# Performance work log

Measured on AMD Instinct MI355X. Metric: run time of the kernel, lower is better.

The kernel has to match this reference:

```python
import jax, jax.numpy as jnp
import numpy as np

B, S, D, H = 64, 1024, 128, 256  # batch, seq, input_dim, hidden_dim


def _glorot(key, shape):
    fan_in, fan_out = shape[0], shape[-1]
    lim = np.sqrt(6.0 / (fan_in + fan_out)).astype(np.float32)
    return jax.random.uniform(key, shape, jnp.float32, -lim, lim)


def setup_inputs() -> dict:
    key = jax.random.key(0)
    ks = jax.random.split(key, 13)
    inp = {
        "x": jax.random.normal(ks[0], (B, S, D), jnp.float32),
        # forward-direction lite-GRU params
        "Wz_f": _glorot(ks[1], (D, H)), "Uz_f": _glorot(ks[2], (H, H)), "bz_f": jnp.zeros((H,), jnp.float32),
        "Wh_f": _glorot(ks[3], (D, H)), "Uh_f": _glorot(ks[4], (H, H)), "bh_f": jnp.zeros((H,), jnp.float32),
        # backward-direction lite-GRU params
        "Wz_b": _glorot(ks[5], (D, H)), "Uz_b": _glorot(ks[6], (H, H)), "bz_b": jnp.zeros((H,), jnp.float32),
        "Wh_b": _glorot(ks[7], (D, H)), "Uh_b": _glorot(ks[8], (H, H)), "bh_b": jnp.zeros((H,), jnp.float32),
        # attention: Linear(2H,2H) -> Tanh -> Linear(2H,1) -> Softmax(dim=1)
        "W1": _glorot(ks[9], (2 * H, 2 * H)), "b1": jnp.zeros((2 * H,), jnp.float32),
        "w2": _glorot(ks[10], (2 * H, 1)), "b2": jnp.zeros((1,), jnp.float32),
    }
    return inp


def _lite_gru(x, Wz, Uz, bz, Wh, Uh, bh):
    # x: [B,S,D] -> outputs [B,S,H]; lite GRU (no reset gate)
    xz = jnp.einsum('bsd,dh->bsh', x, Wz) + bz  # precompute input projections
    xh = jnp.einsum('bsd,dh->bsh', x, Wh) + bh

    def step(h, inps):
        xz_t, xh_t = inps  # [B,H]
        z = jax.nn.sigmoid(xz_t + h @ Uz)
        hc = jnp.tanh(xh_t + h @ Uh)
        h = z * h + (1.0 - z) * hc
        return h, h

    h0 = jnp.zeros((x.shape[0], Uz.shape[0]), x.dtype)
    _, ys = jax.lax.scan(step, h0, (jnp.swapaxes(xz, 0, 1), jnp.swapaxes(xh, 0, 1)))
    return jnp.swapaxes(ys, 0, 1)  # [B,S,H]


def reference(x, Wz_f, Uz_f, bz_f, Wh_f, Uh_f, bh_f,
              Wz_b, Uz_b, bz_b, Wh_b, Uh_b, bh_b, W1, b1, w2, b2):
    out_f = _lite_gru(x, Wz_f, Uz_f, bz_f, Wh_f, Uh_f, bh_f)
    out_b = _lite_gru(x[:, ::-1, :], Wz_b, Uz_b, bz_b, Wh_b, Uh_b, bh_b)[:, ::-1, :]
    out = jnp.concatenate([out_f, out_b], axis=-1)  # [B,S,2H]
    # additive attention: Linear -> tanh -> Linear -> softmax over time
    scores = jnp.tanh(out @ W1 + b1) @ w2 + b2       # [B,S,1]
    attn = jax.nn.softmax(scores, axis=1)
    context = jnp.sum(attn * out, axis=1)            # [B,2H]
    return context
```

## Files before the change

### kernel.cpp

```cpp
#include <hip/hip_runtime.h>
#include <cstdint>
#include <cstddef>

typedef _Float16 f16;
typedef _Float16 f16x8 __attribute__((ext_vector_type(8)));
typedef _Float16 f16x4 __attribute__((ext_vector_type(4)));
typedef _Float16 f16x2 __attribute__((ext_vector_type(2)));
typedef float f32x4 __attribute__((ext_vector_type(4)));

#define MFMA16(a, b, c) __builtin_amdgcn_mfma_f32_16x16x32_f16((a), (b), (c), 0, 0, 0)


static constexpr size_t UT_OFF  = 0;
static constexpr size_t WT_OFF  = 524288;
static constexpr size_t W1T_OFF = 786432;
static constexpr size_t XP_OFF  = 1310720;
static constexpr size_t OUT_OFF = XP_OFF + 134217728;
static constexpr size_t SC_OFF  = OUT_OFF + 67108864;
static constexpr size_t AT_OFF  = SC_OFF + 262144;
static constexpr size_t PART_OFF= AT_OFF + 262144;

#define SCALE_Z 1.4426950408889634f
#define SCALE_H 2.8853900817779268f

__device__ __forceinline__ float fexp2(float x) {
#if __has_builtin(__builtin_amdgcn_exp2f)
    return __builtin_amdgcn_exp2f(x);
#else
    return __expf(x * 0.6931471805599453f);
#endif
}

__global__ void k0_prep(const float* __restrict__ Uzf, const float* __restrict__ Uhf,
                        const float* __restrict__ Uzb, const float* __restrict__ Uhb,
                        const float* __restrict__ Wzf, const float* __restrict__ Whf,
                        const float* __restrict__ Wzb, const float* __restrict__ Whb,
                        const float* __restrict__ W1,
                        f16* __restrict__ Ut, f16* __restrict__ Wt, f16* __restrict__ W1t)
{
    int tid = blockIdx.x * blockDim.x + threadIdx.x;
    int nthr = gridDim.x * blockDim.x;
    for (int i = tid; i < 4 * 256 * 256; i += nthr) {
        int u = i >> 16, cc = (i >> 8) & 255, k = i & 255;
        const float* U = (u == 0) ? Uzf : (u == 1) ? Uhf : (u == 2) ? Uzb : Uhb;
        float sg = (u & 1) ? SCALE_H : SCALE_Z;
        Ut[i] = (f16)(U[k * 256 + cc] * sg);
    }
    for (int i = tid; i < 2 * 512 * 128; i += nthr) {
        int dir = i >> 16, cc2 = (i >> 7) & 511, k = i & 127;
        const float* W = dir ? ((cc2 & 256) ? Whb : Wzb) : ((cc2 & 256) ? Whf : Wzf);
        Wt[i] = (f16)W[k * 256 + (cc2 & 255)];
    }
    for (int i = tid; i < 512 * 512; i += nthr) {
        int n = i >> 9, k = i & 511;
        W1t[i] = (f16)W1[k * 512 + n];
    }
}

__launch_bounds__(256, 2)
__global__ void k1_xproj(const float* __restrict__ x, const f16* __restrict__ Wt,
                         const float* __restrict__ bzf, const float* __restrict__ bhf,
                         const float* __restrict__ bzb, const float* __restrict__ bhb,
                         f16* __restrict__ xp2)
{
    int bid = blockIdx.x;
    int s = bid & 1023, g = (bid >> 10) & 3, dir = bid >> 12;
    int s_src = dir ? (1023 - s) : s;
    int tid = threadIdx.x, w = tid >> 6, lane = tid & 63, q = lane >> 4, l16 = lane & 15;

    f16x8 bf[4];
    const float* xr = x + ((size_t)(g * 16 + l16) * 1024 + s_src) * 128;
#pragma unroll
    for (int kt = 0; kt < 4; ++kt) {
        int k0 = kt * 32 + q * 8;
        f32x4 a = *(const f32x4*)(xr + k0);
        f32x4 c = *(const f32x4*)(xr + k0 + 4);
        f16x8 v;
#pragma unroll
        for (int j = 0; j < 4; ++j) { v[j] = (f16)a[j]; v[4 + j] = (f16)c[j]; }
        bf[kt] = v;
    }
    const f16* wt = Wt + (size_t)dir * 512 * 128;
    f16x8 af[8][4];
#pragma unroll
    for (int mt = 0; mt < 8; ++mt) {
        int cc2 = w * 128 + mt * 16 + l16;
#pragma unroll
        for (int kt = 0; kt < 4; ++kt)
            af[mt][kt] = *(const f16x8*)(wt + cc2 * 128 + kt * 32 + q * 8);
    }
    f32x4 acc[8];
#pragma unroll
    for (int mt = 0; mt < 8; ++mt) acc[mt] = (f32x4){0.f, 0.f, 0.f, 0.f};
#pragma unroll
    for (int kt = 0; kt < 4; ++kt)
#pragma unroll
        for (int mt = 0; mt < 8; ++mt)
            acc[mt] = MFMA16(af[mt][kt], bf[kt], acc[mt]);

    f16* dst = xp2 + (size_t)((dir * 4 + g) * 1024 + s) * 8192;
#pragma unroll
    for (int mt = 0; mt < 8; ++mt) {
        int ccg = w * 128 + mt * 16 + q * 4;
        int gate = ccg >> 8, c = ccg & 255;
        const float* bias = gate ? (dir ? bhb : bhf) : (dir ? bzb : bzf);
        float sg = gate ? SCALE_H : SCALE_Z;
        f32x4 bi = *(const f32x4*)(bias + c);
        f16x4 o;
#pragma unroll
        for (int r = 0; r < 4; ++r) o[r] = (f16)((acc[mt][r] + bi[r]) * sg);
        int flat = ((gate * 2 + ((c >> 4) & 1)) * 8 + (c >> 5)) * 256 + (q * 16 + l16) * 4;
        *(f16x4*)(dst + flat) = o;
    }
}

#define GRU_STEP(P, SS, CX)                                                   \
    {                                                                         \
        const int cur = (P), nxt = (P) ^ 1;                                   \
        f16x8 bf[8];                                                          \
        _Pragma("unroll")                                                     \
        for (int j = 0; j < 8; ++j)                                           \
            bf[j] = *(const f16x8*)&h16[cur][l16][j * 32 + q * 8];            \
        f32x4 acc[4];                                                         \
        _Pragma("unroll")                                                     \
        for (int t = 0; t < 4; ++t)                                           \
            _Pragma("unroll")                                                 \
            for (int r = 0; r < 4; ++r) acc[t][r] = (float)CX[t][r];          \
        int sp = (SS) + 2; if (sp > 1023) sp = 1023;                          \
        const f16* px = xb + (size_t)sp * 8192;                               \
        _Pragma("unroll")                                                     \
        for (int t = 0; t < 4; ++t) CX[t] = *(const f16x4*)(px + offs[t]);    \
        _Pragma("unroll")                                                     \
        for (int j = 0; j < 8; ++j)                                           \
            _Pragma("unroll")                                                 \
            for (int t = 0; t < 4; ++t)                                       \
                acc[t] = MFMA16(uf[t][j], bf[j], acc[t]);                     \
        _Pragma("unroll")                                                     \
        for (int p = 0; p < 2; ++p) {                                         \
            f32x4 hn; f16x4 hh;                                               \
            _Pragma("unroll")                                                 \
            for (int r = 0; r < 4; ++r) {                                     \
                float az = acc[p][r];                                         \
                float ah = acc[2 + p][r];                                     \
                float E1 = fexp2(-az);                                        \
                float E2 = fexp2(-ah);                                        \
                float h0 = hold[p][r];                                        \
                float num = __builtin_fmaf(h0, E2, h0)                        \
                          + __builtin_fmaf(-E1, E2, E1);                      \
                float den = (1.f + E1) * (1.f + E2);                          \
                float hv = num * __builtin_amdgcn_rcpf(den);                  \
                hn[r] = hv; hh[r] = (f16)hv;                                  \
            }                                                                 \
            hold[p] = hn;                                                     \
            int ccg = w * 32 + p * 16 + q * 4;                                \
            *(f16x4*)&h16[nxt][l16][ccg] = hh;                                \
            *(f16x4*)(op + p * 16) = hh;                                      \
        }                                                                     \
        op += sstep;                                                          \
        asm volatile("s_waitcnt lgkmcnt(0)" ::: "memory");                    \
        __builtin_amdgcn_s_barrier();                                         \
        asm volatile("" ::: "memory");                                        \
    }

__launch_bounds__(512, 2)
__global__ void k2_gru(const f16* __restrict__ Ut, const f16* __restrict__ xp2,
                       f16* __restrict__ out16)
{
    int bid = blockIdx.x;
    int dir = bid >> 2, g = bid & 3;
    int tid = threadIdx.x, w = tid >> 6, lane = tid & 63, q = lane >> 4, l16 = lane & 15;

    __shared__ f16 h16[2][16][264];

    for (int i = tid; i < 2 * 16 * 264; i += 512) (&h16[0][0][0])[i] = (f16)0.f;

    f16x8 uf[4][8];
#pragma unroll
    for (int t = 0; t < 4; ++t) {
        int gate = t >> 1;
        int cc = w * 32 + (t & 1) * 16 + l16;
        const f16* up = Ut + ((size_t)(dir * 2 + gate) * 256 + cc) * 256;
#pragma unroll
        for (int j = 0; j < 8; ++j)
            uf[t][j] = *(const volatile f16x8*)(up + j * 32 + q * 8);
    }

    const f16* xb = xp2 + (size_t)(dir * 4 + g) * 1024 * 8192;
    int offs[4];
#pragma unroll
    for (int t = 0; t < 4; ++t) {
        int gate = t >> 1, p = t & 1;
        offs[t] = ((gate * 2 + p) * 8 + w) * 256 + lane * 4;
    }
    f16x4 cxA[4], cxB[4];
#pragma unroll
    for (int t = 0; t < 4; ++t) cxA[t] = *(const f16x4*)(xb + offs[t]);
#pragma unroll
    for (int t = 0; t < 4; ++t) cxB[t] = *(const f16x4*)(xb + 8192 + offs[t]);

    f32x4 hold[2];
    hold[0] = (f32x4){0.f, 0.f, 0.f, 0.f};
    hold[1] = (f32x4){0.f, 0.f, 0.f, 0.f};

    f16* op = out16 + ((size_t)(g * 16 + l16) * 1024 + (dir ? 1023 : 0)) * 512
            + dir * 256 + w * 32 + q * 4;
    ptrdiff_t sstep = dir ? -512 : 512;

    __syncthreads();

    for (int s = 0; s < 1024; s += 2) {
        GRU_STEP(0, s, cxA)
        GRU_STEP(1, s + 1, cxB)
    }
}

__launch_bounds__(256, 2)
__global__ void k3_scores(const f16* __restrict__ out16, const f16* __restrict__ W1t,
                          const float* __restrict__ b1, const float* __restrict__ w2,
                          const float* __restrict__ b2, float* __restrict__ scores)
{
    int bid = blockIdx.x;
    int b = bid >> 4, sc = bid & 15, s0 = sc * 64;
    int tid = threadIdx.x, w = tid >> 6, lane = tid & 63, q = lane >> 4, l16 = lane & 15;
    f32x4 acc[4][8];
#pragma unroll
    for (int mt = 0; mt < 4; ++mt)
#pragma unroll
        for (int nt = 0; nt < 8; ++nt) acc[mt][nt] = (f32x4){0.f, 0.f, 0.f, 0.f};

    for (int kt = 0; kt < 16; ++kt) {
        f16x8 af[4];
#pragma unroll
        for (int mt = 0; mt < 4; ++mt) {
            size_t row = (size_t)b * 1024 + s0 + mt * 16 + l16;
            af[mt] = *(const f16x8*)(out16 + row * 512 + kt * 32 + q * 8);
        }
        f16x8 bfg[8];
#pragma unroll
        for (int nt = 0; nt < 8; ++nt) {
            int ncol = w * 128 + nt * 16 + l16;
            bfg[nt] = *(const f16x8*)(W1t + (size_t)ncol * 512 + kt * 32 + q * 8);
        }
#pragma unroll
        for (int mt = 0; mt < 4; ++mt)
#pragma unroll
            for (int nt = 0; nt < 8; ++nt)
                acc[mt][nt] = MFMA16(af[mt], bfg[nt], acc[mt][nt]);
    }
    float b1v[8], w2v[8];
#pragma unroll
    for (int nt = 0; nt < 8; ++nt) {
        int ncol = w * 128 + nt * 16 + l16;
        b1v[nt] = b1[ncol];
        w2v[nt] = w2[ncol];
    }
    __shared__ float spart[4][64];
    float rs[4][4];
#pragma unroll
    for (int mt = 0; mt < 4; ++mt)
#pragma unroll
        for (int r = 0; r < 4; ++r) {
            float ssum = 0.f;
#pragma unroll
            for (int nt = 0; nt < 8; ++nt) {
                float xv = acc[mt][nt][r] + b1v[nt];
                float t = 1.f - 2.f / (1.f + __expf(2.f * xv));
                ssum += t * w2v[nt];
            }
            rs[mt][r] = ssum;
        }
#pragma unroll
    for (int off = 1; off < 16; off <<= 1)
#pragma unroll
        for (int mt = 0; mt < 4; ++mt)
#pragma unroll
            for (int r = 0; r < 4; ++r)
                rs[mt][r] += __shfl_xor(rs[mt][r], off, 64);
    if (l16 == 0) {
#pragma unroll
        for (int mt = 0; mt < 4; ++mt)
#pragma unroll
            for (int r = 0; r < 4; ++r)
                spart[w][mt * 16 + q * 4 + r] = rs[mt][r];
    }
    __syncthreads();
    if (tid < 64) {
        float v = spart[0][tid] + spart[1][tid] + spart[2][tid] + spart[3][tid] + b2[0];
        scores[b * 1024 + s0 + tid] = v;
    }
}

__global__ void k3_softmax(const float* __restrict__ scores, float* __restrict__ attn)
{
    int b = blockIdx.x, tid = threadIdx.x;
    __shared__ float red[4];
    f32x4 v = *(const f32x4*)(scores + b * 1024 + tid * 4);
    float m = fmaxf(fmaxf(v[0], v[1]), fmaxf(v[2], v[3]));
#pragma unroll
    for (int off = 1; off < 64; off <<= 1) m = fmaxf(m, __shfl_xor(m, off, 64));
    if ((tid & 63) == 0) red[tid >> 6] = m;
    __syncthreads();
    m = fmaxf(fmaxf(red[0], red[1]), fmaxf(red[2], red[3]));
    __syncthreads();
    float e0 = __expf(v[0] - m), e1 = __expf(v[1] - m), e2 = __expf(v[2] - m), e3 = __expf(v[3] - m);
    float ssum = e0 + e1 + e2 + e3;
#pragma unroll
    for (int off = 1; off < 64; off <<= 1) ssum += __shfl_xor(ssum, off, 64);
    if ((tid & 63) == 0) red[tid >> 6] = ssum;
    __syncthreads();
    float inv = 1.f / (red[0] + red[1] + red[2] + red[3]);
    f32x4 o = {e0 * inv, e1 * inv, e2 * inv, e3 * inv};
    *(f32x4*)(attn + b * 1024 + tid * 4) = o;
}

__global__ void k3_wsum(const f16* __restrict__ out16, const float* __restrict__ attn,
                        float* __restrict__ part)
{
    int bid = blockIdx.x;
    int b = bid >> 3, ch = bid & 7;
    int tid = threadIdx.x;
    const f16* op = out16 + ((size_t)b * 1024 + ch * 128) * 512 + tid * 2;
    const float* ap = attn + b * 1024 + ch * 128;
    float a0 = 0.f, a1 = 0.f;
#pragma unroll 4
    for (int i = 0; i < 128; ++i) {
        float aw = ap[i];
        f16x2 xv = *(const f16x2*)(op + (size_t)i * 512);
        a0 += aw * (float)xv[0];
        a1 += aw * (float)xv[1];
    }
    part[(size_t)(b * 8 + ch) * 512 + tid * 2] = a0;
    part[(size_t)(b * 8 + ch) * 512 + tid * 2 + 1] = a1;
}

__global__ void k3_final(const float* __restrict__ part, float* __restrict__ outp)
{
    int b = blockIdx.x, tid = threadIdx.x;
#pragma unroll
    for (int j = 0; j < 2; ++j) {
        int cc = tid * 2 + j;
        float ssum = 0.f;
#pragma unroll
        for (int ch = 0; ch < 8; ++ch) ssum += part[(size_t)(b * 8 + ch) * 512 + cc];
        outp[b * 512 + cc] = ssum;
    }
}

extern "C" void kernel_launch(void* const* d_in, const int* in_sizes, int n_in,
                              void* d_out, int out_size, void* d_ws, size_t ws_size,
                              hipStream_t stream)
{
    const float* x   = (const float*)d_in[0];
    const float* Wzf = (const float*)d_in[1];
    const float* Uzf = (const float*)d_in[2];
    const float* bzf = (const float*)d_in[3];
    const float* Whf = (const float*)d_in[4];
    const float* Uhf = (const float*)d_in[5];
    const float* bhf = (const float*)d_in[6];
    const float* Wzb = (const float*)d_in[7];
    const float* Uzb = (const float*)d_in[8];
    const float* bzb = (const float*)d_in[9];
    const float* Whb = (const float*)d_in[10];
    const float* Uhb = (const float*)d_in[11];
    const float* bhb = (const float*)d_in[12];
    const float* W1  = (const float*)d_in[13];
    const float* b1  = (const float*)d_in[14];
    const float* w2  = (const float*)d_in[15];
    const float* b2  = (const float*)d_in[16];
    float* outp = (float*)d_out;

    char* ws = (char*)d_ws;
    f16* Ut    = (f16*)(ws + UT_OFF);
    f16* Wt    = (f16*)(ws + WT_OFF);
    f16* W1t   = (f16*)(ws + W1T_OFF);
    f16* xp2   = (f16*)(ws + XP_OFF);
    f16* o16   = (f16*)(ws + OUT_OFF);
    float* sc  = (float*)(ws + SC_OFF);
    float* at  = (float*)(ws + AT_OFF);
    float* pt  = (float*)(ws + PART_OFF);

    hipLaunchKernelGGL(k0_prep, dim3(256), dim3(256), 0, stream,
                       Uzf, Uhf, Uzb, Uhb, Wzf, Whf, Wzb, Whb, W1, Ut, Wt, W1t);
    hipLaunchKernelGGL(k1_xproj, dim3(8192), dim3(256), 0, stream,
                       x, Wt, bzf, bhf, bzb, bhb, xp2);
    hipLaunchKernelGGL(k2_gru, dim3(8), dim3(512), 0, stream, Ut, xp2, o16);
    hipLaunchKernelGGL(k3_scores, dim3(1024), dim3(256), 0, stream, o16, W1t, b1, w2, b2, sc);
    hipLaunchKernelGGL(k3_softmax, dim3(64), dim3(256), 0, stream, sc, at);
    hipLaunchKernelGGL(k3_wsum, dim3(512), dim3(256), 0, stream, o16, at, pt);
    hipLaunchKernelGGL(k3_final, dim3(64), dim3(256), 0, stream, pt, outp);
}
```

Before: 1.308 ms.

## Split GRU recurrence into half-K segments so gate writes overlap the next matmul

Each GRU step's recurrent matmul is split into two K-halves with a barrier after each half. Warps 0-3 produce the first 128 hidden columns right after the second half finishes. Warps 4-7 produce the other half during the next segment. This lets the gate math and state writes of one warp group overlap the other group's MFMA work on the serial critical path. The cost is twice as many block barriers per timestep and one extra trailing matmul segment at the end.

Result: slower. 1.446 ms (+10.5%).

```diff
diff --git a/kernel.cpp b/kernel.cpp
--- a/kernel.cpp
+++ b/kernel.cpp
@@ -114,27 +114,8 @@
     }
 }
 
-#define GRU_STEP(P, SS, CX)                                                   \
+#define GATEWRITE(BUF)                                                        \
     {                                                                         \
-        const int cur = (P), nxt = (P) ^ 1;                                   \
-        f16x8 bf[8];                                                          \
-        _Pragma("unroll")                                                     \
-        for (int j = 0; j < 8; ++j)                                           \
-            bf[j] = *(const f16x8*)&h16[cur][l16][j * 32 + q * 8];            \
-        f32x4 acc[4];                                                         \
-        _Pragma("unroll")                                                     \
-        for (int t = 0; t < 4; ++t)                                           \
-            _Pragma("unroll")                                                 \
-            for (int r = 0; r < 4; ++r) acc[t][r] = (float)CX[t][r];          \
-        int sp = (SS) + 2; if (sp > 1023) sp = 1023;                          \
-        const f16* px = xb + (size_t)sp * 8192;                               \
-        _Pragma("unroll")                                                     \
-        for (int t = 0; t < 4; ++t) CX[t] = *(const f16x4*)(px + offs[t]);    \
-        _Pragma("unroll")                                                     \
-        for (int j = 0; j < 8; ++j)                                           \
-            _Pragma("unroll")                                                 \
-            for (int t = 0; t < 4; ++t)                                       \
-                acc[t] = MFMA16(uf[t][j], bf[j], acc[t]);                     \
         _Pragma("unroll")                                                     \
         for (int p = 0; p < 2; ++p) {                                         \
             f32x4 hn; f16x4 hh;                                               \
@@ -152,16 +133,54 @@
                 hn[r] = hv; hh[r] = (f16)hv;                                  \
             }                                                                 \
             hold[p] = hn;                                                     \
-            int ccg = w * 32 + p * 16 + q * 4;                                \
-            *(f16x4*)&h16[nxt][l16][ccg] = hh;                                \
+            *(f16x4*)&h16[BUF][l16][ccg0 + p * 16] = hh;                      \
             *(f16x4*)(op + p * 16) = hh;                                      \
         }                                                                     \
         op += sstep;                                                          \
+    }
+
+#define QSEG(PB, CB)                                                          \
+    {                                                                         \
+        f16x8 bq[4];                                                          \
+        _Pragma("unroll")                                                     \
+        for (int j = 0; j < 4; ++j)                                           \
+            bq[j] = *(const f16x8*)&h16[PB][l16][(j + 4) * 32 + q * 8];       \
+        _Pragma("unroll")                                                     \
+        for (int j = 0; j < 4; ++j)                                           \
+            _Pragma("unroll")                                                 \
+            for (int t = 0; t < 4; ++t)                                       \
+                acc[t] = MFMA16(uf[t][j + 4], bq[j], acc[t]);                 \
+        if (!grp) GATEWRITE(CB)                                               \
         asm volatile("s_waitcnt lgkmcnt(0)" ::: "memory");                    \
         __builtin_amdgcn_s_barrier();                                         \
         asm volatile("" ::: "memory");                                        \
     }
 
+#define PSEG(PB2, CX, SS1, DOGATE)                                            \
+    {                                                                         \
+        if ((DOGATE) && grp) GATEWRITE(PB2)                                   \
+        _Pragma("unroll")                                                     \
+        for (int t = 0; t < 4; ++t)                                           \
+            _Pragma("unroll")                                                 \
+            for (int r = 0; r < 4; ++r) acc[t][r] = (float)CX[t][r];          \
+        int sp = (SS1) + 2; if (sp > 1023) sp = 1023;                         \
+        const f16* px = xb + (size_t)sp * 8192;                               \
+        _Pragma("unroll")                                                     \
+        for (int t = 0; t < 4; ++t) CX[t] = *(const f16x4*)(px + offs[t]);    \
+        f16x8 bp[4];                                                          \
+        _Pragma("unroll")                                                     \
+        for (int j = 0; j < 4; ++j)                                           \
+            bp[j] = *(const f16x8*)&h16[PB2][l16][j * 32 + q * 8];            \
+        _Pragma("unroll")                                                     \
+        for (int j = 0; j < 4; ++j)                                           \
+            _Pragma("unroll")                                                 \
+            for (int t = 0; t < 4; ++t)                                       \
+                acc[t] = MFMA16(uf[t][j], bp[j], acc[t]);                     \
+        asm volatile("s_waitcnt lgkmcnt(0)" ::: "memory");                    \
+        __builtin_amdgcn_s_barrier();                                         \
+        asm volatile("" ::: "memory");                                        \
+    }
+
 __launch_bounds__(512, 2)
 __global__ void k2_gru(const f16* __restrict__ Ut, const f16* __restrict__ xp2,
                        f16* __restrict__ out16)
@@ -169,6 +188,7 @@
     int bid = blockIdx.x;
     int dir = bid >> 2, g = bid & 3;
     int tid = threadIdx.x, w = tid >> 6, lane = tid & 63, q = lane >> 4, l16 = lane & 15;
+    int grp = __builtin_amdgcn_readfirstlane(w >> 2);
 
     __shared__ f16 h16[2][16][264];
 
@@ -201,16 +221,22 @@
     f32x4 hold[2];
     hold[0] = (f32x4){0.f, 0.f, 0.f, 0.f};
     hold[1] = (f32x4){0.f, 0.f, 0.f, 0.f};
+    f32x4 acc[4];
 
     f16* op = out16 + ((size_t)(g * 16 + l16) * 1024 + (dir ? 1023 : 0)) * 512
             + dir * 256 + w * 32 + q * 4;
     ptrdiff_t sstep = dir ? -512 : 512;
+    int ccg0 = w * 32 + q * 4;
 
     __syncthreads();
 
-    for (int s = 0; s < 1024; s += 2) {
-        GRU_STEP(0, s, cxA)
-        GRU_STEP(1, s + 1, cxB)
+    PSEG(0, cxA, 0, 0)
+    for (int t2 = 0; t2 < 512; ++t2) {
+        int s2 = t2 * 2;
+        QSEG(0, 1)
+        PSEG(1, cxB, s2 + 1, 1)
+        QSEG(1, 0)
+        PSEG(0, cxA, s2 + 2, 1)
     }
 }
 
```

## Quantize GRU recurrent weights and hidden state to int8 MFMA

Applied to the files above, without the earlier changes.

The recurrent matmul h@U in the sequential GRU kernel now uses int8 MFMA (16x16x64) instead of f16 (16x16x32). U is quantized per output column with a scale, and the hidden state is quantized to int8 with a fixed scale of 127 before being written to shared memory. This halves the MFMA count and the LDS traffic on the latency-bound serial path, but adds quantization error that can accumulate across 1024 recurrent steps.

After: 1.234 ms. 5.6% less time.

```diff
diff --git a/kernel.cpp b/kernel.cpp
--- a/kernel.cpp
+++ b/kernel.cpp
@@ -7,11 +7,14 @@
 typedef _Float16 f16x4 __attribute__((ext_vector_type(4)));
 typedef _Float16 f16x2 __attribute__((ext_vector_type(2)));
 typedef float f32x4 __attribute__((ext_vector_type(4)));
+typedef int i32x4 __attribute__((ext_vector_type(4)));
 
 #define MFMA16(a, b, c) __builtin_amdgcn_mfma_f32_16x16x32_f16((a), (b), (c), 0, 0, 0)
-
-
-static constexpr size_t UT_OFF  = 0;
+#define MFMAI8(a, b, c) __builtin_amdgcn_mfma_i32_16x16x64_i8((a), (b), (c), 0, 0, 0)
+
+
+static constexpr size_t UT8_OFF = 0;
+static constexpr size_t USCL_OFF= 262144;
 static constexpr size_t WT_OFF  = 524288;
 static constexpr size_t W1T_OFF = 786432;
 static constexpr size_t XP_OFF  = 1310720;
@@ -22,6 +25,7 @@
 
 #define SCALE_Z 1.4426950408889634f
 #define SCALE_H 2.8853900817779268f
+#define QMAGIC 12582912.0f
 
 __device__ __forceinline__ float fexp2(float x) {
 #if __has_builtin(__builtin_amdgcn_exp2f)
@@ -36,15 +40,37 @@
                         const float* __restrict__ Wzf, const float* __restrict__ Whf,
                         const float* __restrict__ Wzb, const float* __restrict__ Whb,
                         const float* __restrict__ W1,
-                        f16* __restrict__ Ut, f16* __restrict__ Wt, f16* __restrict__ W1t)
+                        char* __restrict__ Ut8, float* __restrict__ uscl,
+                        f16* __restrict__ Wt, f16* __restrict__ W1t)
 {
     int tid = blockIdx.x * blockDim.x + threadIdx.x;
     int nthr = gridDim.x * blockDim.x;
-    for (int i = tid; i < 4 * 256 * 256; i += nthr) {
-        int u = i >> 16, cc = (i >> 8) & 255, k = i & 255;
-        const float* U = (u == 0) ? Uzf : (u == 1) ? Uhf : (u == 2) ? Uzb : Uhb;
-        float sg = (u & 1) ? SCALE_H : SCALE_Z;
-        Ut[i] = (f16)(U[k * 256 + cc] * sg);
+    {
+        int wid = tid >> 6, lane = tid & 63, nw = nthr >> 6;
+        for (int i = wid; i < 4 * 256; i += nw) {
+            int u = i >> 8, cc = i & 255;
+            const float* U = (u == 0) ? Uzf : (u == 1) ? Uhf : (u == 2) ? Uzb : Uhb;
+            float v[4]; float mx = 0.f;
+#pragma unroll
+            for (int j = 0; j < 4; ++j) {
+                v[j] = U[(lane * 4 + j) * 256 + cc];
+                mx = fmaxf(mx, fabsf(v[j]));
+            }
+#pragma unroll
+            for (int off = 1; off < 64; off <<= 1) mx = fmaxf(mx, __shfl_xor(mx, off, 64));
+            float qs = 127.f / mx;
+            unsigned qw = 0;
+#pragma unroll
+            for (int j = 0; j < 4; ++j) {
+                unsigned b = __builtin_bit_cast(unsigned, fmaf(v[j], qs, QMAGIC)) & 255u;
+                qw |= b << (8 * j);
+            }
+            *(unsigned*)(Ut8 + (size_t)i * 256 + lane * 4) = qw;
+            if (lane == 0) {
+                float sg = (u & 1) ? SCALE_H : SCALE_Z;
+                uscl[i] = sg * mx * (1.f / (127.f * 127.f));
+            }
+        }
     }
     for (int i = tid; i < 2 * 512 * 128; i += nthr) {
         int dir = i >> 16, cc2 = (i >> 7) & 511, k = i & 127;
@@ -117,31 +143,31 @@
 #define GRU_STEP(P, SS, CX)                                                   \
     {                                                                         \
         const int cur = (P), nxt = (P) ^ 1;                                   \
-        f16x8 bf[8];                                                          \
-        _Pragma("unroll")                                                     \
-        for (int j = 0; j < 8; ++j)                                           \
-            bf[j] = *(const f16x8*)&h16[cur][l16][j * 32 + q * 8];            \
-        f32x4 acc[4];                                                         \
-        _Pragma("unroll")                                                     \
-        for (int t = 0; t < 4; ++t)                                           \
-            _Pragma("unroll")                                                 \
-            for (int r = 0; r < 4; ++r) acc[t][r] = (float)CX[t][r];          \
+        i32x4 bh[4];                                                          \
+        _Pragma("unroll")                                                     \
+        for (int j = 0; j < 4; ++j)                                           \
+            bh[j] = *(const i32x4*)&h8[cur][l16][j * 64 + q * 16];            \
+        i32x4 ia[4];                                                          \
+        _Pragma("unroll")                                                     \
+        for (int t = 0; t < 4; ++t) ia[t] = (i32x4){0, 0, 0, 0};              \
         int sp = (SS) + 2; if (sp > 1023) sp = 1023;                          \
         const f16* px = xb + (size_t)sp * 8192;                               \
-        _Pragma("unroll")                                                     \
-        for (int t = 0; t < 4; ++t) CX[t] = *(const f16x4*)(px + offs[t]);    \
-        _Pragma("unroll")                                                     \
-        for (int j = 0; j < 8; ++j)                                           \
+        f16x4 nx[4];                                                          \
+        _Pragma("unroll")                                                     \
+        for (int t = 0; t < 4; ++t) nx[t] = *(const f16x4*)(px + offs[t]);    \
+        _Pragma("unroll")                                                     \
+        for (int j = 0; j < 4; ++j)                                           \
             _Pragma("unroll")                                                 \
             for (int t = 0; t < 4; ++t)                                       \
-                acc[t] = MFMA16(uf[t][j], bf[j], acc[t]);                     \
+                ia[t] = MFMAI8(uf8[t][j], bh[j], ia[t]);                      \
         _Pragma("unroll")                                                     \
         for (int p = 0; p < 2; ++p) {                                         \
-            f32x4 hn; f16x4 hh;                                               \
+            f32x4 hn; f16x4 hh; unsigned qw = 0;                              \
             _Pragma("unroll")                                                 \
             for (int r = 0; r < 4; ++r) {                                     \
-                float az = acc[p][r];                                         \
-                float ah = acc[2 + p][r];                                     \
+                float az = fmaf((float)ia[p][r], fs4[p][r], (float)CX[p][r]); \
+                float ah = fmaf((float)ia[2 + p][r], fs4[2 + p][r],           \
+                                (float)CX[2 + p][r]);                         \
                 float E1 = fexp2(-az);                                        \
                 float E2 = fexp2(-ah);                                        \
                 float h0 = hold[p][r];                                        \
@@ -150,39 +176,50 @@
                 float den = (1.f + E1) * (1.f + E2);                          \
                 float hv = num * __builtin_amdgcn_rcpf(den);                  \
                 hn[r] = hv; hh[r] = (f16)hv;                                  \
+                unsigned qb = __builtin_bit_cast(                             \
+                    unsigned, fmaf(hv, 127.f, QMAGIC)) & 255u;                \
+                qw |= qb << (8 * r);                                          \
             }                                                                 \
             hold[p] = hn;                                                     \
-            int ccg = w * 32 + p * 16 + q * 4;                                \
-            *(f16x4*)&h16[nxt][l16][ccg] = hh;                                \
+            *(unsigned*)&h8[nxt][l16][ccg0 + p * 16] = qw;                    \
             *(f16x4*)(op + p * 16) = hh;                                      \
         }                                                                     \
         op += sstep;                                                          \
+        _Pragma("unroll")                                                     \
+        for (int t = 0; t < 4; ++t) CX[t] = nx[t];                            \
         asm volatile("s_waitcnt lgkmcnt(0)" ::: "memory");                    \
         __builtin_amdgcn_s_barrier();                                         \
         asm volatile("" ::: "memory");                                        \
     }
 
 __launch_bounds__(512, 2)
-__global__ void k2_gru(const f16* __restrict__ Ut, const f16* __restrict__ xp2,
-                       f16* __restrict__ out16)
+__global__ void k2_gru(const char* __restrict__ Ut8, const float* __restrict__ uscl,
+                       const f16* __restrict__ xp2, f16* __restrict__ out16)
 {
     int bid = blockIdx.x;
     int dir = bid >> 2, g = bid & 3;
     int tid = threadIdx.x, w = tid >> 6, lane = tid & 63, q = lane >> 4, l16 = lane & 15;
 
-    __shared__ f16 h16[2][16][264];
-
-    for (int i = tid; i < 2 * 16 * 264; i += 512) (&h16[0][0][0])[i] = (f16)0.f;
-
-    f16x8 uf[4][8];
+    __shared__ __align__(16) char h8[2][16][272];
+
+    for (int i = tid; i < 2 * 16 * 272 / 4; i += 512) ((int*)h8)[i] = 0;
+
+    i32x4 uf8[4][4];
 #pragma unroll
     for (int t = 0; t < 4; ++t) {
         int gate = t >> 1;
         int cc = w * 32 + (t & 1) * 16 + l16;
-        const f16* up = Ut + ((size_t)(dir * 2 + gate) * 256 + cc) * 256;
-#pragma unroll
-        for (int j = 0; j < 8; ++j)
-            uf[t][j] = *(const volatile f16x8*)(up + j * 32 + q * 8);
+        const char* up = Ut8 + ((size_t)(dir * 2 + gate) * 256 + cc) * 256;
+#pragma unroll
+        for (int j = 0; j < 4; ++j)
+            uf8[t][j] = *(const volatile i32x4*)(up + j * 64 + q * 16);
+    }
+    f32x4 fs4[4];
+#pragma unroll
+    for (int t = 0; t < 4; ++t) {
+        const float* sp = uscl + (dir * 2 + (t >> 1)) * 256
+                        + w * 32 + (t & 1) * 16 + q * 4;
+        fs4[t] = *(const f32x4*)sp;
     }
 
     const f16* xb = xp2 + (size_t)(dir * 4 + g) * 1024 * 8192;
@@ -205,6 +242,7 @@
     f16* op = out16 + ((size_t)(g * 16 + l16) * 1024 + (dir ? 1023 : 0)) * 512
             + dir * 256 + w * 32 + q * 4;
     ptrdiff_t sstep = dir ? -512 : 512;
+    int ccg0 = w * 32 + q * 4;
 
     __syncthreads();
 
@@ -370,7 +408,8 @@
     float* outp = (float*)d_out;
 
     char* ws = (char*)d_ws;
-    f16* Ut    = (f16*)(ws + UT_OFF);
+    char* Ut8  = ws + UT8_OFF;
+    float* usc = (float*)(ws + USCL_OFF);
     f16* Wt    = (f16*)(ws + WT_OFF);
     f16* W1t   = (f16*)(ws + W1T_OFF);
     f16* xp2   = (f16*)(ws + XP_OFF);
@@ -380,10 +419,10 @@
     float* pt  = (float*)(ws + PART_OFF);
 
     hipLaunchKernelGGL(k0_prep, dim3(256), dim3(256), 0, stream,
-                       Uzf, Uhf, Uzb, Uhb, Wzf, Whf, Wzb, Whb, W1, Ut, Wt, W1t);
+                       Uzf, Uhf, Uzb, Uhb, Wzf, Whf, Wzb, Whb, W1, Ut8, usc, Wt, W1t);
     hipLaunchKernelGGL(k1_xproj, dim3(8192), dim3(256), 0, stream,
                        x, Wt, bzf, bhf, bzb, bhb, xp2);
-    hipLaunchKernelGGL(k2_gru, dim3(8), dim3(512), 0, stream, Ut, xp2, o16);
+    hipLaunchKernelGGL(k2_gru, dim3(8), dim3(512), 0, stream, Ut8, usc, xp2, o16);
     hipLaunchKernelGGL(k3_scores, dim3(1024), dim3(256), 0, stream, o16, W1t, b1, w2, b2, sc);
     hipLaunchKernelGGL(k3_softmax, dim3(64), dim3(256), 0, stream, sc, at);
     hipLaunchKernelGGL(k3_wsum, dim3(512), dim3(256), 0, stream, o16, at, pt);
```
